# Kernel optimization log

Measured on AMD Instinct MI355X. Metric: run time of the kernel, lower is better.

The kernel has to match this reference:

```python
import jax, jax.numpy as jnp
import numpy as np

IN_DIM, H1, H2, N_CLASSES = 128, 100, 128, 19
BATCH, SEQ = 512, 256


def _lstm_relu(x, W, U, b, units):
    """Keras LSTM with activation='relu', recurrent_activation='sigmoid'.
    x: [B, T, D]. Returns (all hidden states [B, T, units], last hidden [B, units]).
    Gate order (Keras): i, f, g(cell candidate), o.
    """
    B = x.shape[0]
    h0 = jnp.zeros((B, units), x.dtype)
    c0 = jnp.zeros((B, units), x.dtype)

    # precompute input projections for all timesteps: [T, B, 4*units]
    zx = jnp.einsum('btd,dk->tbk', x, W) + b

    def step(carry, zx_t):
        h, c = carry
        z = zx_t + h @ U
        i, f, g, o = jnp.split(z, 4, axis=-1)
        i = jax.nn.sigmoid(i)
        f = jax.nn.sigmoid(f)
        g = jax.nn.relu(g)          # activation='relu'
        o = jax.nn.sigmoid(o)
        c = f * c + i * g
        h = o * jax.nn.relu(c)      # output activation is also relu
        return (h, c), h

    (h_last, _), hs = jax.lax.scan(step, (h0, c0), zx)
    return jnp.transpose(hs, (1, 0, 2)), h_last


def setup_inputs() -> dict:
    key = jax.random.key(0)
    ks = jax.random.split(key, 9)
    def w(k, shape, fan_in):
        return jax.random.normal(k, shape, jnp.float32) / np.sqrt(fan_in)
    x = jax.random.normal(ks[0], (BATCH, SEQ, IN_DIM), jnp.float32)
    return {
        'x': x,
        'W1': w(ks[1], (IN_DIM, 4 * H1), IN_DIM),
        'U1': w(ks[2], (H1, 4 * H1), H1),
        'b1': jnp.zeros((4 * H1,), jnp.float32),
        'W2': w(ks[3], (H1, 4 * H2), H1),
        'U2': w(ks[4], (H2, 4 * H2), H2),
        'b2': jnp.zeros((4 * H2,), jnp.float32),
        'Wd': w(ks[5], (H2, N_CLASSES), H2),
        'bd': jnp.zeros((N_CLASSES,), jnp.float32),
    }


def reference(x, W1, U1, b1, W2, U2, b2, Wd, bd):
    h1_seq, _ = _lstm_relu(x, W1, U1, b1, H1)      # [B, T, 100]
    _, h2 = _lstm_relu(h1_seq, W2, U2, b2, H2)     # [B, 128] (last step only)
    logits = h2 @ Wd + bd
    return jax.nn.softmax(logits, axis=-1)         # [B, 19]
```

## Files before the change

### kernel.cpp

```cpp
#include <hip/hip_runtime.h>
#include <math.h>


#define T_SEQ 256
#define BATCH 512
#define IN_DIM 128
#define H1 100
#define H2 128
#define NCLS 19

typedef float f4v __attribute__((ext_vector_type(4)));

__device__ __forceinline__ float sigmoidf_(float x) {
    return 1.0f / (1.0f + __expf(-x));
}
__device__ __forceinline__ float hsum4_(f4v v) {
    return (v.x + v.y) + (v.z + v.w);
}

#define REP8(M)  M(0) M(1) M(2) M(3) M(4) M(5) M(6) M(7)
#define REP25(M) M(0) M(1) M(2) M(3) M(4) M(5) M(6) M(7) M(8) M(9) M(10) M(11) \
                 M(12) M(13) M(14) M(15) M(16) M(17) M(18) M(19) M(20) M(21) M(22) M(23) M(24)

template<int K, int N, bool SWAP>
__global__ __launch_bounds__(256, 2)
void proj_kernel(const float* __restrict__ A, const float* __restrict__ W,
                 const float* __restrict__ bias, float* __restrict__ out)
{
    constexpr int LD = 132;
    __shared__ __align__(16) float As[32 * LD];
    __shared__ __align__(16) float Ws[32 * LD];
    const int tid = threadIdx.x;
    const int r0 = blockIdx.x * 128;
    const int c0 = blockIdx.y * 128;
    const int ty = tid >> 4, tx = tid & 15;

#define PACC(i) f4v accL##i = {0.f,0.f,0.f,0.f}; f4v accR##i = {0.f,0.f,0.f,0.f};
    REP8(PACC)
#undef PACC

    for (int kk = 0; kk < K; kk += 32) {
        __syncthreads();
#pragma unroll
        for (int i = 0; i < 4; ++i) {
            int idx = tid + i * 256;
            int row = idx >> 3, kg = idx & 7;
            int k = kk + kg * 4;
            f4v v = {0.f, 0.f, 0.f, 0.f};
            if (k < K) v = *(const f4v*)&A[(size_t)(r0 + row) * K + k];
            As[(kg * 4 + 0) * LD + row] = v.x;
            As[(kg * 4 + 1) * LD + row] = v.y;
            As[(kg * 4 + 2) * LD + row] = v.z;
            As[(kg * 4 + 3) * LD + row] = v.w;
        }
#pragma unroll
        for (int i = 0; i < 4; ++i) {
            int idx = tid + i * 256;
            int k = idx >> 5, cg = idx & 31;
            int gk = kk + k, gc = c0 + cg * 4;
            f4v v = {0.f, 0.f, 0.f, 0.f};
            if (gk < K && gc < N) v = *(const f4v*)&W[(size_t)gk * N + gc];
            *(f4v*)&Ws[k * LD + cg * 4] = v;
        }
        __syncthreads();
#pragma unroll
        for (int k = 0; k < 32; ++k) {
            f4v av0 = *(const f4v*)&As[k * LD + ty * 8];
            f4v av1 = *(const f4v*)&As[k * LD + ty * 8 + 4];
            f4v b0v = *(const f4v*)&Ws[k * LD + tx * 8];
            f4v b1v = *(const f4v*)&Ws[k * LD + tx * 8 + 4];
#define PFMA(i, s) accL##i += (s) * b0v; accR##i += (s) * b1v;
            PFMA(0, av0.x) PFMA(1, av0.y) PFMA(2, av0.z) PFMA(3, av0.w)
            PFMA(4, av1.x) PFMA(5, av1.y) PFMA(6, av1.z) PFMA(7, av1.w)
#undef PFMA
        }
    }

    const int cb = c0 + tx * 8;
    float b0 = (cb + 0 < N) ? bias[cb + 0] : 0.f;
    float b1 = (cb + 1 < N) ? bias[cb + 1] : 0.f;
    float b2 = (cb + 2 < N) ? bias[cb + 2] : 0.f;
    float b3 = (cb + 3 < N) ? bias[cb + 3] : 0.f;
    float b4 = (cb + 4 < N) ? bias[cb + 4] : 0.f;
    float b5 = (cb + 5 < N) ? bias[cb + 5] : 0.f;
    float b6 = (cb + 6 < N) ? bias[cb + 6] : 0.f;
    float b7 = (cb + 7 < N) ? bias[cb + 7] : 0.f;
    f4v bL = {b0, b1, b2, b3};
    f4v bR = {b4, b5, b6, b7};
#define PST(i) { \
        int r = r0 + ty * 8 + i; \
        size_t orow = SWAP ? ((size_t)(r & 255) * BATCH + (r >> 8)) : (size_t)r; \
        if (cb < N)     { f4v v = accL##i + bL; *(f4v*)&out[orow * N + cb] = v; } \
        if (cb + 4 < N) { f4v v = accR##i + bR; *(f4v*)&out[orow * N + cb + 4] = v; } }
    REP8(PST)
#undef PST
}

__global__ __launch_bounds__(256)
__attribute__((amdgpu_waves_per_eu(1, 1)))
void rec1_kernel(const float* __restrict__ zx,
                 const float* __restrict__ U1,
                 float* __restrict__ h1seq)
{
    const int row = blockIdx.x;
    const int k = threadIdx.x;
    __shared__ __align__(16) float hs[H1];
    __shared__ __align__(8) float fo[2 * H1];

    const int kk = (k < 200) ? k : 0;
    const int c0 = kk, c1 = kk + 200;

#define R1_LD(i) \
    f4v u0_##i, u1_##i; { \
        const float* p = U1 + (4 * i) * 400; \
        u0_##i = (f4v){p[c0], p[400 + c0], p[800 + c0], p[1200 + c0]}; \
        u1_##i = (f4v){p[c1], p[400 + c1], p[800 + c1], p[1200 + c1]}; }
    REP25(R1_LD)
#undef R1_LD

    if (k < H1) hs[k] = 0.0f;
    float cst = 0.0f;
    float zc0 = zx[(size_t)row * 400 + c0];
    float zc1 = zx[(size_t)row * 400 + c1];
    __syncthreads();

    for (int t = 0; t < T_SEQ; ++t) {
        int tn = (t + 1 < T_SEQ) ? t + 1 : t;
        const float* pz = &zx[((size_t)tn * BATCH + row) * 400];
        float zn0 = pz[c0];
        float zn1 = pz[c1];

        f4v s0 = {0.f, 0.f, 0.f, 0.f};
        f4v s1 = {0.f, 0.f, 0.f, 0.f};
#define R1_FMA(i) { f4v hv = *(const f4v*)&hs[4 * i]; s0 += hv * u0_##i; s1 += hv * u1_##i; }
        REP25(R1_FMA)
#undef R1_FMA
        float a0 = sigmoidf_(zc0 + hsum4_(s0));
        float a1h = zc1 + hsum4_(s1);
        float a1 = (k < H1) ? fmaxf(a1h, 0.0f) : sigmoidf_(a1h);
        if (k >= H1 && k < 200) *(float2*)&fo[2 * (k - H1)] = make_float2(a0, a1);
        __syncthreads();

        if (k < H1) {
            float2 f_o = *(const float2*)&fo[2 * k];
            cst = f_o.x * cst + a0 * a1;
            float h = f_o.y * fmaxf(cst, 0.0f);
            hs[k] = h;
            h1seq[((size_t)t * BATCH + row) * H1 + k] = h;
        }
        __syncthreads();
        zc0 = zn0;
        zc1 = zn1;
    }
}

template<bool INIT, bool LAST>
__global__ __launch_bounds__(512)
__attribute__((amdgpu_waves_per_eu(2, 2)))
void rec2_chunk(const float* __restrict__ zx,
                const float* __restrict__ U2,
                float* __restrict__ cbuf,
                float* __restrict__ hbuf,
                float* __restrict__ h2out,
                int tlen)
{
    const int row = blockIdx.x;
    const int tid = threadIdx.x;
    const int kq = tid >> 7;
    const int cl = tid & 127;
    __shared__ __align__(16) float hs[H2];
    __shared__ float zp[4 * 512];
    __shared__ float za[512];

#define R2_LD(j) \
    f4v w0_##j, w1_##j, w2_##j, w3_##j; { \
        const float* p = U2 + (size_t)(kq * 32 + 4 * j) * 512 + cl; \
        w0_##j = (f4v){p[0],   p[512],       p[1024],       p[1536]}; \
        w1_##j = (f4v){p[128], p[512 + 128], p[1024 + 128], p[1536 + 128]}; \
        w2_##j = (f4v){p[256], p[512 + 256], p[1024 + 256], p[1536 + 256]}; \
        w3_##j = (f4v){p[384], p[512 + 384], p[1024 + 384], p[1536 + 384]}; }
    REP8(R2_LD)
#undef R2_LD

    float cst = 0.0f;
    if (tid < H2) {
        if (INIT) {
            hs[tid] = 0.0f;
        } else {
            hs[tid] = hbuf[(size_t)row * H2 + tid];
            cst = cbuf[(size_t)row * H2 + tid];
        }
    }
    float zc = zx[(size_t)row * 512 + tid];
    __syncthreads();

    for (int t = 0; t < tlen; ++t) {
        int tn = (t + 1 < tlen) ? t + 1 : t;
        float zn = zx[((size_t)tn * BATCH + row) * 512 + tid];

        f4v s0 = {0.f, 0.f, 0.f, 0.f};
        f4v s1 = {0.f, 0.f, 0.f, 0.f};
        f4v s2 = {0.f, 0.f, 0.f, 0.f};
        f4v s3 = {0.f, 0.f, 0.f, 0.f};
#define R2_FMA(j) { f4v hv = *(const f4v*)&hs[kq * 32 + 4 * j]; \
        s0 += hv * w0_##j; s1 += hv * w1_##j; s2 += hv * w2_##j; s3 += hv * w3_##j; }
        REP8(R2_FMA)
#undef R2_FMA
        zp[kq * 512 + cl]       = hsum4_(s0);
        zp[kq * 512 + cl + 128] = hsum4_(s1);
        zp[kq * 512 + cl + 256] = hsum4_(s2);
        zp[kq * 512 + cl + 384] = hsum4_(s3);
        __syncthreads();

        float z = zc + (zp[tid] + zp[512 + tid]) + (zp[1024 + tid] + zp[1536 + tid]);
        float a = (tid >= 2 * H2 && tid < 3 * H2) ? fmaxf(z, 0.0f) : sigmoidf_(z);
        za[tid] = a;
        __syncthreads();

        if (tid < H2) {
            float i = za[tid], f = za[tid + 128], g = za[tid + 256], o = za[tid + 384];
            cst = f * cst + i * g;
            hs[tid] = o * fmaxf(cst, 0.0f);
        }
        __syncthreads();
        zc = zn;
    }

    if (tid < H2) {
        float h = hs[tid];
        cbuf[(size_t)row * H2 + tid] = cst;
        hbuf[(size_t)row * H2 + tid] = h;
        if (LAST) h2out[(size_t)row * H2 + tid] = h;
    }
}

__global__ __launch_bounds__(64, 1)
void dense_softmax_kernel(const float* __restrict__ h2, const float* __restrict__ Wd,
                          const float* __restrict__ bd, float* __restrict__ out)
{
    const int b = blockIdx.x;
    const int k = threadIdx.x;
    __shared__ __align__(16) float hsm[H2];
    if (k < H2 / 4) ((f4v*)hsm)[k] = ((const f4v*)(h2 + (size_t)b * H2))[k];
    __syncthreads();

    float logit = -1e30f;
    if (k < NCLS) {
        float acc = bd[k];
#pragma unroll
        for (int d = 0; d < H2; ++d) acc += hsm[d] * Wd[d * NCLS + k];
        logit = acc;
    }
    float m = logit;
#pragma unroll
    for (int off = 32; off >= 1; off >>= 1) m = fmaxf(m, __shfl_xor(m, off, 64));
    float e = (k < NCLS) ? __expf(logit - m) : 0.0f;
    float s = e;
#pragma unroll
    for (int off = 32; off >= 1; off >>= 1) s += __shfl_xor(s, off, 64);
    if (k < NCLS) out[(size_t)b * NCLS + k] = e / s;
}

__global__ __launch_bounds__(448, 1)
void lstm1_fb(const float* __restrict__ x, const float* __restrict__ W1,
              const float* __restrict__ U1, const float* __restrict__ b1,
              float* __restrict__ h1out)
{
    const int b = blockIdx.x;
    const int k = threadIdx.x;
    __shared__ __align__(16) float xs[IN_DIM];
    __shared__ __align__(16) float hs[H1];
    __shared__ __align__(16) float zs[4 * H1];
    float w1r[IN_DIM];
    float u1r[H1];
    float bias = 0.0f;
    if (k < 4 * H1) {
        bias = b1[k];
#pragma unroll
        for (int d = 0; d < IN_DIM; ++d) w1r[d] = W1[d * (4 * H1) + k];
#pragma unroll
        for (int j = 0; j < H1; ++j) u1r[j] = U1[j * (4 * H1) + k];
    }
    if (k < H1) hs[k] = 0.0f;
    if (k < IN_DIM / 4)
        ((float4*)xs)[k] = ((const float4*)(x + ((size_t)b * T_SEQ) * IN_DIM))[k];
    float c = 0.0f;
    __syncthreads();
    for (int t = 0; t < T_SEQ; ++t) {
        if (k < 4 * H1) {
            float acc0 = bias, acc1 = 0.f, acc2 = 0.f, acc3 = 0.f;
#pragma unroll
            for (int q = 0; q < IN_DIM / 4; ++q) {
                float4 xv = ((const float4*)xs)[q];
                acc0 += xv.x * w1r[4 * q]; acc1 += xv.y * w1r[4 * q + 1];
                acc2 += xv.z * w1r[4 * q + 2]; acc3 += xv.w * w1r[4 * q + 3];
            }
#pragma unroll
            for (int q = 0; q < H1 / 4; ++q) {
                float4 hv = ((const float4*)hs)[q];
                acc0 += hv.x * u1r[4 * q]; acc1 += hv.y * u1r[4 * q + 1];
                acc2 += hv.z * u1r[4 * q + 2]; acc3 += hv.w * u1r[4 * q + 3];
            }
            float zv = (acc0 + acc1) + (acc2 + acc3);
            zs[k] = (k >= 2 * H1 && k < 3 * H1) ? fmaxf(zv, 0.0f) : sigmoidf_(zv);
        }
        __syncthreads();
        if (k < H1) {
            float i = zs[k], f = zs[k + H1], g = zs[k + 2 * H1], o = zs[k + 3 * H1];
            c = f * c + i * g;
            float h = o * fmaxf(c, 0.0f);
            hs[k] = h;
            h1out[((size_t)t * BATCH + b) * H1 + k] = h;
        }
        int tn = t + 1;
        if (tn < T_SEQ && k < IN_DIM / 4)
            ((float4*)xs)[k] = ((const float4*)(x + ((size_t)b * T_SEQ + tn) * IN_DIM))[k];
        __syncthreads();
    }
}

__global__ __launch_bounds__(512, 1)
void lstm2_fb(const float* __restrict__ h1in, const float* __restrict__ W2,
              const float* __restrict__ U2, const float* __restrict__ b2,
              float* __restrict__ h2out)
{
    const int b = blockIdx.x;
    const int k = threadIdx.x;
    __shared__ __align__(16) float ps[H1];
    __shared__ __align__(16) float hs[H2];
    __shared__ __align__(16) float zs[4 * H2];
    float w2r[H1];
    float u2r[H2];
    float bias = b2[k];
#pragma unroll
    for (int j = 0; j < H1; ++j) w2r[j] = W2[j * (4 * H2) + k];
#pragma unroll
    for (int j = 0; j < H2; ++j) u2r[j] = U2[j * (4 * H2) + k];
    if (k < H2) hs[k] = 0.0f;
    if (k < H1 / 4)
        ((float4*)ps)[k] = ((const float4*)(h1in + (size_t)b * H1))[k];
    float c = 0.0f;
    float hlast = 0.0f;
    __syncthreads();
    for (int t = 0; t < T_SEQ; ++t) {
        float acc0 = bias, acc1 = 0.f, acc2 = 0.f, acc3 = 0.f;
#pragma unroll
        for (int q = 0; q < H1 / 4; ++q) {
            float4 pv = ((const float4*)ps)[q];
            acc0 += pv.x * w2r[4 * q]; acc1 += pv.y * w2r[4 * q + 1];
            acc2 += pv.z * w2r[4 * q + 2]; acc3 += pv.w * w2r[4 * q + 3];
        }
#pragma unroll
        for (int q = 0; q < H2 / 4; ++q) {
            float4 hv = ((const float4*)hs)[q];
            acc0 += hv.x * u2r[4 * q]; acc1 += hv.y * u2r[4 * q + 1];
            acc2 += hv.z * u2r[4 * q + 2]; acc3 += hv.w * u2r[4 * q + 3];
        }
        float zv = (acc0 + acc1) + (acc2 + acc3);
        zs[k] = (k >= 2 * H2 && k < 3 * H2) ? fmaxf(zv, 0.0f) : sigmoidf_(zv);
        __syncthreads();
        if (k < H2) {
            float i = zs[k], f = zs[k + H2], g = zs[k + 2 * H2], o = zs[k + 3 * H2];
            c = f * c + i * g;
            hlast = o * fmaxf(c, 0.0f);
            hs[k] = hlast;
        }
        int tn = t + 1;
        if (tn < T_SEQ && k < H1 / 4)
            ((float4*)ps)[k] = ((const float4*)(h1in + ((size_t)tn * BATCH + b) * H1))[k];
        __syncthreads();
    }
    if (k < H2) h2out[(size_t)b * H2 + k] = hlast;
}

extern "C" void kernel_launch(void* const* d_in, const int* in_sizes, int n_in,
                              void* d_out, int out_size, void* d_ws, size_t ws_size,
                              hipStream_t stream) {
    const float* x  = (const float*)d_in[0];
    const float* W1 = (const float*)d_in[1];
    const float* U1 = (const float*)d_in[2];
    const float* b1 = (const float*)d_in[3];
    const float* W2 = (const float*)d_in[4];
    const float* U2 = (const float*)d_in[5];
    const float* b2 = (const float*)d_in[6];
    const float* Wd = (const float*)d_in[7];
    const float* bd = (const float*)d_in[8];
    float* out = (float*)d_out;

    const size_t zx_elems = (size_t)T_SEQ * BATCH * 400;
    const size_t h1_elems = (size_t)T_SEQ * BATCH * H1;
    const size_t st_elems = (size_t)BATCH * H2;
    const size_t need = (zx_elems + h1_elems + 3 * st_elems) * sizeof(float);

    if (ws_size >= need) {
        float* zxbuf = (float*)d_ws;
        float* h1buf = zxbuf + zx_elems;
        float* cbuf  = h1buf + h1_elems;
        float* hbuf  = cbuf + st_elems;
        float* h2buf = hbuf + st_elems;
        const int TC = T_SEQ / 2;

        hipLaunchKernelGGL((proj_kernel<IN_DIM, 4 * H1, true>), dim3(1024, 4), dim3(256), 0, stream,
                           x, W1, b1, zxbuf);
        hipLaunchKernelGGL(rec1_kernel, dim3(BATCH), dim3(256), 0, stream,
                           zxbuf, U1, h1buf);
        hipLaunchKernelGGL((proj_kernel<H1, 4 * H2, false>), dim3(512, 4), dim3(256), 0, stream,
                           h1buf, W2, b2, zxbuf);
        hipLaunchKernelGGL((rec2_chunk<true, false>), dim3(BATCH), dim3(512), 0, stream,
                           zxbuf, U2, cbuf, hbuf, h2buf, TC);
        hipLaunchKernelGGL((proj_kernel<H1, 4 * H2, false>), dim3(512, 4), dim3(256), 0, stream,
                           h1buf + (size_t)TC * BATCH * H1, W2, b2, zxbuf);
        hipLaunchKernelGGL((rec2_chunk<false, true>), dim3(BATCH), dim3(512), 0, stream,
                           zxbuf, U2, cbuf, hbuf, h2buf, TC);

        hipLaunchKernelGGL(dense_softmax_kernel, dim3(BATCH), dim3(64), 0, stream,
                           h2buf, Wd, bd, out);
    } else {
        float* h1buf = (float*)d_ws;
        float* h2buf = h1buf + h1_elems;
        hipLaunchKernelGGL(lstm1_fb, dim3(BATCH), dim3(448), 0, stream, x, W1, U1, b1, h1buf);
        hipLaunchKernelGGL(lstm2_fb, dim3(BATCH), dim3(512), 0, stream, h1buf, W2, U2, b2, h2buf);
        hipLaunchKernelGGL(dense_softmax_kernel, dim3(BATCH), dim3(64), 0, stream, h2buf, Wd, bd, out);
    }
}
```

Before: 1.384 ms.

## Process two batch rows per block in layer-1 recurrence kernel

The first LSTM recurrence kernel now handles two batch rows per workgroup and launches half as many blocks. Each thread reuses its register-resident U1 weights for both rows, which doubles the independent FMA work per barrier and halves the per-block weight loading. In exchange each timestep has a longer serial chain per block, and with only 256 blocks there are fewer workgroups to spread across the GPU's compute units.

```diff
diff --git a/kernel.cpp b/kernel.cpp
--- a/kernel.cpp
+++ b/kernel.cpp
@@ -102,10 +102,13 @@
                  const float* __restrict__ U1,
                  float* __restrict__ h1seq)
 {
-    const int row = blockIdx.x;
+    const int rowA = blockIdx.x * 2;
+    const int rowB = rowA + 1;
     const int k = threadIdx.x;
-    __shared__ __align__(16) float hs[H1];
-    __shared__ __align__(8) float fo[2 * H1];
+    __shared__ __align__(16) float hsA[H1];
+    __shared__ __align__(16) float hsB[H1];
+    __shared__ __align__(8) float foA[2 * H1];
+    __shared__ __align__(8) float foB[2 * H1];
 
     const int kk = (k < 200) ? k : 0;
     const int c0 = kk, c1 = kk + 200;
@@ -118,39 +121,61 @@
     REP25(R1_LD)
 #undef R1_LD
 
-    if (k < H1) hs[k] = 0.0f;
-    float cst = 0.0f;
-    float zc0 = zx[(size_t)row * 400 + c0];
-    float zc1 = zx[(size_t)row * 400 + c1];
+    if (k < H1) { hsA[k] = 0.0f; hsB[k] = 0.0f; }
+    float cstA = 0.0f, cstB = 0.0f;
+    float zcA0 = zx[(size_t)rowA * 400 + c0];
+    float zcA1 = zx[(size_t)rowA * 400 + c1];
+    float zcB0 = zx[(size_t)rowB * 400 + c0];
+    float zcB1 = zx[(size_t)rowB * 400 + c1];
     __syncthreads();
 
     for (int t = 0; t < T_SEQ; ++t) {
         int tn = (t + 1 < T_SEQ) ? t + 1 : t;
-        const float* pz = &zx[((size_t)tn * BATCH + row) * 400];
-        float zn0 = pz[c0];
-        float zn1 = pz[c1];
-
-        f4v s0 = {0.f, 0.f, 0.f, 0.f};
-        f4v s1 = {0.f, 0.f, 0.f, 0.f};
-#define R1_FMA(i) { f4v hv = *(const f4v*)&hs[4 * i]; s0 += hv * u0_##i; s1 += hv * u1_##i; }
+        const float* pzA = &zx[((size_t)tn * BATCH + rowA) * 400];
+        const float* pzB = &zx[((size_t)tn * BATCH + rowB) * 400];
+        float znA0 = pzA[c0];
+        float znA1 = pzA[c1];
+        float znB0 = pzB[c0];
+        float znB1 = pzB[c1];
+
+        f4v sA0 = {0.f, 0.f, 0.f, 0.f};
+        f4v sA1 = {0.f, 0.f, 0.f, 0.f};
+        f4v sB0 = {0.f, 0.f, 0.f, 0.f};
+        f4v sB1 = {0.f, 0.f, 0.f, 0.f};
+#define R1_FMA(i) { \
+        f4v hvA = *(const f4v*)&hsA[4 * i]; \
+        f4v hvB = *(const f4v*)&hsB[4 * i]; \
+        sA0 += hvA * u0_##i; sA1 += hvA * u1_##i; \
+        sB0 += hvB * u0_##i; sB1 += hvB * u1_##i; }
         REP25(R1_FMA)
 #undef R1_FMA
-        float a0 = sigmoidf_(zc0 + hsum4_(s0));
-        float a1h = zc1 + hsum4_(s1);
-        float a1 = (k < H1) ? fmaxf(a1h, 0.0f) : sigmoidf_(a1h);
-        if (k >= H1 && k < 200) *(float2*)&fo[2 * (k - H1)] = make_float2(a0, a1);
+        float aA0 = sigmoidf_(zcA0 + hsum4_(sA0));
+        float aB0 = sigmoidf_(zcB0 + hsum4_(sB0));
+        float aA1h = zcA1 + hsum4_(sA1);
+        float aB1h = zcB1 + hsum4_(sB1);
+        float aA1 = (k < H1) ? fmaxf(aA1h, 0.0f) : sigmoidf_(aA1h);
+        float aB1 = (k < H1) ? fmaxf(aB1h, 0.0f) : sigmoidf_(aB1h);
+        if (k >= H1 && k < 200) {
+            *(float2*)&foA[2 * (k - H1)] = make_float2(aA0, aA1);
+            *(float2*)&foB[2 * (k - H1)] = make_float2(aB0, aB1);
+        }
         __syncthreads();
 
         if (k < H1) {
-            float2 f_o = *(const float2*)&fo[2 * k];
-            cst = f_o.x * cst + a0 * a1;
-            float h = f_o.y * fmaxf(cst, 0.0f);
-            hs[k] = h;
-            h1seq[((size_t)t * BATCH + row) * H1 + k] = h;
-        }
-        __syncthreads();
-        zc0 = zn0;
-        zc1 = zn1;
+            float2 foAv = *(const float2*)&foA[2 * k];
+            float2 foBv = *(const float2*)&foB[2 * k];
+            cstA = foAv.x * cstA + aA0 * aA1;
+            cstB = foBv.x * cstB + aB0 * aB1;
+            float hA = foAv.y * fmaxf(cstA, 0.0f);
+            float hB = foBv.y * fmaxf(cstB, 0.0f);
+            hsA[k] = hA;
+            hsB[k] = hB;
+            h1seq[((size_t)t * BATCH + rowA) * H1 + k] = hA;
+            h1seq[((size_t)t * BATCH + rowB) * H1 + k] = hB;
+        }
+        __syncthreads();
+        zcA0 = znA0; zcA1 = znA1;
+        zcB0 = znB0; zcB1 = znB1;
     }
 }
 
@@ -402,7 +427,7 @@
 
         hipLaunchKernelGGL((proj_kernel<IN_DIM, 4 * H1, true>), dim3(1024, 4), dim3(256), 0, stream,
                            x, W1, b1, zxbuf);
-        hipLaunchKernelGGL(rec1_kernel, dim3(BATCH), dim3(256), 0, stream,
+        hipLaunchKernelGGL(rec1_kernel, dim3(BATCH / 2), dim3(256), 0, stream,
                            zxbuf, U1, h1buf);
         hipLaunchKernelGGL((proj_kernel<H1, 4 * H2, false>), dim3(512, 4), dim3(256), 0, stream,
                            h1buf, W2, b2, zxbuf);
```

New measurement: 1.318 ms. 4.8% less time.
